# Performance work log

Measured on AMD Instinct MI355X. Metric: run time of the kernel, lower is better.

The kernel has to match this reference:

```python
import jax, jax.numpy as jnp
import numpy as np

BS, R, W, N, H = 256, 4, 128, 2048, 256
TAU, ALPHA, EPS = 1.0, 0.7, 1e-8


def _l2norm(x, axis):
    return x / (jnp.linalg.norm(x, axis=axis, keepdims=True) + EPS)


def _gumbel(u):
    # standard Gumbel(0,1) from uniform samples
    return -jnp.log(-jnp.log(u + 1e-10) + 1e-10)


def setup_inputs() -> dict:
    key = jax.random.key(0)
    ks = jax.random.split(key, 10)
    return {
        "k_r": jax.random.normal(ks[0], (BS, R * W), jnp.float32),
        "m_t": jax.random.normal(ks[1], (BS, W), jnp.float32),
        "hx": jax.random.normal(ks[2], (1, BS, H), jnp.float32),
        "memory": jax.random.uniform(ks[3], (BS, W, N), jnp.float32),
        "usage": jax.random.uniform(ks[4], (BS, N), jnp.float32),
        "read_weights": jax.random.uniform(ks[5], (BS, R, N), jnp.float32),
        "Wg": jax.random.normal(ks[6], (H, 1), jnp.float32) / np.float32(np.sqrt(H)),
        "bg": jnp.zeros((1,), jnp.float32),
        "noise_write": jax.random.uniform(ks[7], (BS, 1, N), jnp.float32),
        "noise_read": jax.random.uniform(ks[8], (BS, R, N), jnp.float32),
        "m_idx": jax.random.randint(ks[9], (BS, N), 0, N).astype(jnp.int64),
        "seq_idx": N,
    }


def reference(k_r, m_t, hx, memory, usage, read_weights, Wg, bg,
              noise_write, noise_read, m_idx, seq_idx):
    # --- key / candidate preprocessing ---
    read_keys = jnp.tanh(k_r.reshape(BS, R, W))   # bs r W
    write_m = jnp.tanh(m_t.reshape(BS, 1, W))     # bs 1 W

    # --- usage bookkeeping (read weights detached as in torch) ---
    u_t = ALPHA * usage + (1.0 - ALPHA) * jax.lax.stop_gradient(read_weights).sum(axis=1)  # bs N

    # --- write (memory-full branch: content-addressed erase/update) ---
    # reversed cosine similarity between candidate and each slot
    dist = jnp.einsum('biw,bwn->bin', _l2norm(write_m, 2), _l2norm(memory, 1))  # bs 1 N
    gamma = jax.nn.sigmoid(hx[-1] @ Wg + bg)                                    # bs 1
    soft_wt = -dist + (gamma * u_t)[:, None, :]                                 # bs 1 N
    write_wt = jax.nn.softmax((1.0 - soft_wt + _gumbel(noise_write)) / TAU, axis=2)  # bs 1 N

    m_erased = jnp.einsum('bin,bwn->biw', write_wt, memory)                     # bs 1 W
    # M * (E - e^T w) + m^T w  with e = ones -> M*(1 - w) + m^T w
    mem_new = memory * (1.0 - write_wt) + jnp.einsum('biw,bin->bwn', write_m, write_wt)
    usage_new = u_t * (1.0 - jax.lax.stop_gradient(write_wt[:, 0, :]))          # bs N

    # --- read (gumbel-softmax content addressing on updated memory) ---
    dist_r = jnp.einsum('brw,bwn->brn', _l2norm(read_keys, 2), _l2norm(mem_new, 1))  # bs r N
    read_wt = jax.nn.softmax((dist_r + _gumbel(noise_read)) / TAU, axis=2)           # bs r N
    m_read = jnp.einsum('brn,bwn->brw', read_wt, mem_new)                            # bs r W

    return (m_read, mem_new, usage_new, read_wt, m_erased)
```

## Files before the change

### kernel.cpp

```cpp
#include <hip/hip_runtime.h>

#define BS   256
#define RR   4
#define WW   128
#define NN   2048
#define HH   256
#define NT   512
#define WH   64
#define NWAVE (NT / 64)
#define RPW  (WH / NWAVE)

typedef float nfloat4 __attribute__((ext_vector_type(4)));

__device__ __forceinline__ float wave_sum(float v) {
#pragma unroll
  for (int m = 32; m >= 1; m >>= 1) v += __shfl_xor(v, m, 64);
  return v;
}
__device__ __forceinline__ float wave_max(float v) {
#pragma unroll
  for (int m = 32; m >= 1; m >>= 1) v = fmaxf(v, __shfl_xor(v, m, 64));
  return v;
}
__device__ __forceinline__ float block_sum(float v, float* s_red) {
  const int tid = threadIdx.x;
  v = wave_sum(v);
  __syncthreads();
  if ((tid & 63) == 0) s_red[tid >> 6] = v;
  __syncthreads();
  float s = s_red[0];
#pragma unroll
  for (int i = 1; i < NWAVE; ++i) s += s_red[i];
  return s;
}
__device__ __forceinline__ float block_max(float v, float* s_red) {
  const int tid = threadIdx.x;
  v = wave_max(v);
  __syncthreads();
  if ((tid & 63) == 0) s_red[tid >> 6] = v;
  __syncthreads();
  float s = s_red[0];
#pragma unroll
  for (int i = 1; i < NWAVE; ++i) s = fmaxf(s, s_red[i]);
  return s;
}
__device__ __forceinline__ void block_max4(float v[RR], float* s_red4) {
  const int tid = threadIdx.x, lane = tid & 63, wid = tid >> 6;
#pragma unroll
  for (int m = 32; m >= 1; m >>= 1) {
#pragma unroll
    for (int r = 0; r < RR; ++r) v[r] = fmaxf(v[r], __shfl_xor(v[r], m, 64));
  }
  __syncthreads();
  if (lane == 0) {
#pragma unroll
    for (int r = 0; r < RR; ++r) s_red4[wid * RR + r] = v[r];
  }
  __syncthreads();
#pragma unroll
  for (int r = 0; r < RR; ++r) {
    float s = s_red4[r];
#pragma unroll
    for (int i = 1; i < NWAVE; ++i) s = fmaxf(s, s_red4[i * RR + r]);
    v[r] = s;
  }
}
__device__ __forceinline__ void block_sum4(float v[RR], float* s_red4) {
  const int tid = threadIdx.x, lane = tid & 63, wid = tid >> 6;
#pragma unroll
  for (int m = 32; m >= 1; m >>= 1) {
#pragma unroll
    for (int r = 0; r < RR; ++r) v[r] += __shfl_xor(v[r], m, 64);
  }
  __syncthreads();
  if (lane == 0) {
#pragma unroll
    for (int r = 0; r < RR; ++r) s_red4[wid * RR + r] = v[r];
  }
  __syncthreads();
#pragma unroll
  for (int r = 0; r < RR; ++r) {
    float s = s_red4[r];
#pragma unroll
    for (int i = 1; i < NWAVE; ++i) s += s_red4[i * RR + r];
    v[r] = s;
  }
}
__device__ __forceinline__ float gumbelf(float u) {
  return -logf(-logf(u + 1e-10f) + 1e-10f);
}

#define STAT(base, rh, comp, b) ((base) + ((size_t)((rh)*6 + (comp)) * BS + (b)) * NN)

__global__ __launch_bounds__(NT, 4) void k1_stats(
    const float* __restrict__ k_r, const float* __restrict__ m_t,
    const float* __restrict__ memory, float* __restrict__ stats)
{
  __shared__ float s_wm[WH];
  __shared__ float s_rk[RR][WH];
  const int bid = blockIdx.x;
  const int b = bid >> 1, rh = bid & 1;
  const int tid = threadIdx.x;
  const int c0 = 4 * tid;

  if (tid < WH) {
    s_wm[tid] = tanhf(m_t[(size_t)b * WW + rh * WH + tid]);
  } else if (tid < WH + RR * WH) {
    const int i = tid - WH;
    s_rk[i >> 6][i & 63] =
        tanhf(k_r[(size_t)b * RR * WW + (i >> 6) * WW + rh * WH + (i & 63)]);
  }
  __syncthreads();

  const float* Mb = memory + (size_t)b * WW * NN + (size_t)rh * WH * NN;
  float cn[4] = {0.f, 0.f, 0.f, 0.f}, wd[4] = {0.f, 0.f, 0.f, 0.f};
  float rdM[RR][4];
#pragma unroll
  for (int r = 0; r < RR; ++r) {
#pragma unroll
    for (int j = 0; j < 4; ++j) rdM[r][j] = 0.f;
  }
#pragma unroll 8
  for (int w = 0; w < WH; ++w) {
    float4 v = *reinterpret_cast<const float4*>(Mb + (size_t)w * NN + c0);
    const float wmw = s_wm[w];
    cn[0] = fmaf(v.x, v.x, cn[0]); wd[0] = fmaf(wmw, v.x, wd[0]);
    cn[1] = fmaf(v.y, v.y, cn[1]); wd[1] = fmaf(wmw, v.y, wd[1]);
    cn[2] = fmaf(v.z, v.z, cn[2]); wd[2] = fmaf(wmw, v.z, wd[2]);
    cn[3] = fmaf(v.w, v.w, cn[3]); wd[3] = fmaf(wmw, v.w, wd[3]);
#pragma unroll
    for (int r = 0; r < RR; ++r) {
      const float rkw = s_rk[r][w];
      rdM[r][0] = fmaf(rkw, v.x, rdM[r][0]);
      rdM[r][1] = fmaf(rkw, v.y, rdM[r][1]);
      rdM[r][2] = fmaf(rkw, v.z, rdM[r][2]);
      rdM[r][3] = fmaf(rkw, v.w, rdM[r][3]);
    }
  }
  float4 o;
  o.x = cn[0]; o.y = cn[1]; o.z = cn[2]; o.w = cn[3];
  *reinterpret_cast<float4*>(STAT(stats, rh, 0, b) + c0) = o;
  o.x = wd[0]; o.y = wd[1]; o.z = wd[2]; o.w = wd[3];
  *reinterpret_cast<float4*>(STAT(stats, rh, 1, b) + c0) = o;
#pragma unroll
  for (int r = 0; r < RR; ++r) {
    o.x = rdM[r][0]; o.y = rdM[r][1]; o.z = rdM[r][2]; o.w = rdM[r][3];
    *reinterpret_cast<float4*>(STAT(stats, rh, 2 + r, b) + c0) = o;
  }
}

__global__ __launch_bounds__(NT) void k2_softmax(
    const float* __restrict__ k_r, const float* __restrict__ m_t,
    const float* __restrict__ hx, const float* __restrict__ usage,
    const float* __restrict__ read_weights, const float* __restrict__ Wg,
    const float* __restrict__ bg, const float* __restrict__ noise_write,
    const float* __restrict__ noise_read, const float* __restrict__ stats,
    float* __restrict__ wt_out, float* __restrict__ usage_new,
    float* __restrict__ read_wt_out)
{
  __shared__ float s_wm[WW];
  __shared__ float s_rk[RR * WW];
  __shared__ float s_red[NWAVE * RR];
  __shared__ float s_rkinv[RR], s_rkwm[RR];

  const int b = blockIdx.x;
  const int tid = threadIdx.x;
  const int lane = tid & 63;
  const int wid = tid >> 6;
  const int c0 = 4 * tid;

  float gp = 0.f;
  if (tid < HH) gp = hx[(size_t)b * HH + tid] * Wg[tid];
  if (tid < WW) s_wm[tid] = tanhf(m_t[(size_t)b * WW + tid]);
  s_rk[tid] = tanhf(k_r[(size_t)b * (RR * WW) + tid]);

  float ut[4];
  {
    const size_t rb = (size_t)b * RR * NN;
    float4 u4 = *reinterpret_cast<const float4*>(usage + (size_t)b * NN + c0);
    float4 r0 = *reinterpret_cast<const float4*>(read_weights + rb + c0);
    float4 r1 = *reinterpret_cast<const float4*>(read_weights + rb + NN + c0);
    float4 r2 = *reinterpret_cast<const float4*>(read_weights + rb + 2 * NN + c0);
    float4 r3 = *reinterpret_cast<const float4*>(read_weights + rb + 3 * NN + c0);
    ut[0] = 0.7f * u4.x + 0.3f * (r0.x + r1.x + r2.x + r3.x);
    ut[1] = 0.7f * u4.y + 0.3f * (r0.y + r1.y + r2.y + r3.y);
    ut[2] = 0.7f * u4.z + 0.3f * (r0.z + r1.z + r2.z + r3.z);
    ut[3] = 0.7f * u4.w + 0.3f * (r0.w + r1.w + r2.w + r3.w);
  }

  const float gamma = 1.f / (1.f + expf(-(block_sum(gp, s_red) + bg[0])));
  float wmp = (tid < WW) ? s_wm[tid] * s_wm[tid] : 0.f;
  const float wmss = block_sum(wmp, s_red);
  const float inv_wm = 1.f / (sqrtf(wmss) + 1e-8f);

  if (wid < RR) {
    const float a = s_rk[wid * WW + lane];
    const float c = s_rk[wid * WW + 64 + lane];
    const float wa = s_wm[lane], wc = s_wm[64 + lane];
    float ss = wave_sum(a * a + c * c);
    float sw = wave_sum(a * wa + c * wc);
    if (lane == 0) {
      s_rkinv[wid] = 1.f / (sqrtf(ss) + 1e-8f);
      s_rkwm[wid] = sw;
    }
  }
  __syncthreads();

  float cn[4], wd[4], rdM[RR][4];
  {
    float4 a0 = *reinterpret_cast<const float4*>(STAT(stats, 0, 0, b) + c0);
    float4 a1 = *reinterpret_cast<const float4*>(STAT(stats, 1, 0, b) + c0);
    cn[0] = a0.x + a1.x; cn[1] = a0.y + a1.y; cn[2] = a0.z + a1.z; cn[3] = a0.w + a1.w;
    float4 b0 = *reinterpret_cast<const float4*>(STAT(stats, 0, 1, b) + c0);
    float4 b1 = *reinterpret_cast<const float4*>(STAT(stats, 1, 1, b) + c0);
    wd[0] = b0.x + b1.x; wd[1] = b0.y + b1.y; wd[2] = b0.z + b1.z; wd[3] = b0.w + b1.w;
#pragma unroll
    for (int r = 0; r < RR; ++r) {
      float4 d0 = *reinterpret_cast<const float4*>(STAT(stats, 0, 2 + r, b) + c0);
      float4 d1 = *reinterpret_cast<const float4*>(STAT(stats, 1, 2 + r, b) + c0);
      rdM[r][0] = d0.x + d1.x; rdM[r][1] = d0.y + d1.y;
      rdM[r][2] = d0.z + d1.z; rdM[r][3] = d0.w + d1.w;
    }
  }

  float lg[4], mx = -1e30f;
  {
    float4 nw = *reinterpret_cast<const float4*>(noise_write + (size_t)b * NN + c0);
    const float nwv[4] = {nw.x, nw.y, nw.z, nw.w};
#pragma unroll
    for (int j = 0; j < 4; ++j) {
      float dist = wd[j] * inv_wm / (sqrtf(cn[j]) + 1e-8f);
      lg[j] = 1.f + dist - gamma * ut[j] + gumbelf(nwv[j]);
      mx = fmaxf(mx, lg[j]);
    }
  }
  mx = block_max(mx, s_red);
  float ex[4], es = 0.f;
#pragma unroll
  for (int j = 0; j < 4; ++j) { ex[j] = expf(lg[j] - mx); es += ex[j]; }
  es = block_sum(es, s_red);
  const float inv_es = 1.f / es;
  float wtk[4], omw[4];
#pragma unroll
  for (int j = 0; j < 4; ++j) { wtk[j] = ex[j] * inv_es; omw[j] = 1.f - wtk[j]; }
  {
    float4 un, wo;
    un.x = ut[0] * omw[0]; un.y = ut[1] * omw[1];
    un.z = ut[2] * omw[2]; un.w = ut[3] * omw[3];
    *reinterpret_cast<float4*>(usage_new + (size_t)b * NN + c0) = un;
    wo.x = wtk[0]; wo.y = wtk[1]; wo.z = wtk[2]; wo.w = wtk[3];
    *reinterpret_cast<float4*>(wt_out + (size_t)b * NN + c0) = wo;
  }

  const float invrk[RR] = { s_rkinv[0], s_rkinv[1], s_rkinv[2], s_rkinv[3] };
  const float rkwm[RR]  = { s_rkwm[0], s_rkwm[1], s_rkwm[2], s_rkwm[3] };
  float inv_cn2[4];
#pragma unroll
  for (int j = 0; j < 4; ++j) {
    float cn2 = omw[j] * omw[j] * cn[j]
              + 2.f * omw[j] * wtk[j] * wd[j]
              + wtk[j] * wtk[j] * wmss;
    inv_cn2[j] = 1.f / (sqrtf(cn2) + 1e-8f);
  }
  float lr[RR][4], mr[RR];
#pragma unroll
  for (int r = 0; r < RR; ++r) {
    float4 nr = *reinterpret_cast<const float4*>(
        noise_read + ((size_t)b * RR + r) * NN + c0);
    const float nrv[4] = {nr.x, nr.y, nr.z, nr.w};
    float m = -1e30f;
#pragma unroll
    for (int j = 0; j < 4; ++j) {
      float rd = omw[j] * rdM[r][j] + wtk[j] * rkwm[r];
      lr[r][j] = rd * invrk[r] * inv_cn2[j] + gumbelf(nrv[j]);
      m = fmaxf(m, lr[r][j]);
    }
    mr[r] = m;
  }
  block_max4(mr, s_red);
  float er[RR][4], ers[RR];
#pragma unroll
  for (int r = 0; r < RR; ++r) {
    float s = 0.f;
#pragma unroll
    for (int j = 0; j < 4; ++j) { er[r][j] = expf(lr[r][j] - mr[r]); s += er[r][j]; }
    ers[r] = s;
  }
  block_sum4(ers, s_red);
#pragma unroll
  for (int r = 0; r < RR; ++r) {
    const float inv_ers = 1.f / ers[r];
    float4 o;
    o.x = er[r][0] * inv_ers; o.y = er[r][1] * inv_ers;
    o.z = er[r][2] * inv_ers; o.w = er[r][3] * inv_ers;
    *reinterpret_cast<float4*>(read_wt_out + ((size_t)b * RR + r) * NN + c0) = o;
  }
}

__global__ __launch_bounds__(NT, 2) void k3_apply(
    const float* __restrict__ m_t, const float* __restrict__ memory,
    const float* __restrict__ wt_in, const float* __restrict__ read_wt,
    float* __restrict__ mem_new, float* __restrict__ m_read,
    float* __restrict__ m_erased)
{
  __shared__ float s_wt[NN];
  __shared__ float s_rwt[RR][NN];

  const int bid = blockIdx.x;
  const int b = bid >> 1, rh = bid & 1;
  const int tid = threadIdx.x;
  const int lane = tid & 63;
  const int wid = tid >> 6;

  {
    const int c = 4 * tid;
    float4 w4 = *reinterpret_cast<const float4*>(wt_in + (size_t)b * NN + c);
    *reinterpret_cast<float4*>(&s_wt[c]) = w4;
#pragma unroll
    for (int r = 0; r < RR; ++r) {
      float4 t = *reinterpret_cast<const float4*>(
          read_wt + ((size_t)b * RR + r) * NN + c);
      *reinterpret_cast<float4*>(&s_rwt[r][c]) = t;
    }
  }
  const int w0 = wid * RPW;
  float wm[RPW];
#pragma unroll
  for (int i = 0; i < RPW; ++i)
    wm[i] = tanhf(m_t[(size_t)b * WW + rh * WH + w0 + i]);
  __syncthreads();

  const size_t hbase = (size_t)b * WW * NN + (size_t)rh * WH * NN;
  const float* Mb = memory + hbase;
  float* MNb = mem_new + hbase;

  float pme[RPW];
  float mrp[RPW][RR];
#pragma unroll
  for (int i = 0; i < RPW; ++i) {
    pme[i] = 0.f;
#pragma unroll
    for (int r = 0; r < RR; ++r) mrp[i][r] = 0.f;
  }

#pragma unroll 1
  for (int ch = 0; ch < NN; ch += 256) {
    const int c = ch + 4 * lane;
    const float4 wt4 = *reinterpret_cast<const float4*>(&s_wt[c]);
    const float ow0 = 1.f - wt4.x, ow1 = 1.f - wt4.y,
                ow2 = 1.f - wt4.z, ow3 = 1.f - wt4.w;
    float4 rw[RR];
#pragma unroll
    for (int r = 0; r < RR; ++r)
      rw[r] = *reinterpret_cast<const float4*>(&s_rwt[r][c]);

#pragma unroll
    for (int i = 0; i < RPW; ++i) {
      const size_t off = (size_t)(w0 + i) * NN + c;
      float4 v = *reinterpret_cast<const float4*>(Mb + off);
      float4 nv;
      nv.x = fmaf(v.x, ow0, wm[i] * wt4.x);
      nv.y = fmaf(v.y, ow1, wm[i] * wt4.y);
      nv.z = fmaf(v.z, ow2, wm[i] * wt4.z);
      nv.w = fmaf(v.w, ow3, wm[i] * wt4.w);
      nfloat4 nvv;
      nvv.x = nv.x; nvv.y = nv.y; nvv.z = nv.z; nvv.w = nv.w;
      __builtin_nontemporal_store(nvv, reinterpret_cast<nfloat4*>(MNb + off));
      float p = wt4.x * v.x;
      p = fmaf(wt4.y, v.y, p);
      p = fmaf(wt4.z, v.z, p);
      p = fmaf(wt4.w, v.w, p);
      pme[i] += p;
#pragma unroll
      for (int r = 0; r < RR; ++r) {
        float a = rw[r].x * nv.x;
        a = fmaf(rw[r].y, nv.y, a);
        a = fmaf(rw[r].z, nv.z, a);
        a = fmaf(rw[r].w, nv.w, a);
        mrp[i][r] += a;
      }
    }
  }

#pragma unroll
  for (int m = 32; m >= 1; m >>= 1) {
#pragma unroll
    for (int i = 0; i < RPW; ++i) {
      pme[i] += __shfl_xor(pme[i], m, 64);
#pragma unroll
      for (int r = 0; r < RR; ++r) mrp[i][r] += __shfl_xor(mrp[i][r], m, 64);
    }
  }
  if (lane == 0) {
    const int wg = rh * WH + w0;
#pragma unroll
    for (int i = 0; i < RPW; ++i) {
      m_erased[(size_t)b * WW + wg + i] = pme[i];
#pragma unroll
      for (int r = 0; r < RR; ++r)
        m_read[(size_t)b * RR * WW + r * WW + wg + i] = mrp[i][r];
    }
  }
}

extern "C" void kernel_launch(void* const* d_in, const int* in_sizes, int n_in,
                              void* d_out, int out_size, void* d_ws, size_t ws_size,
                              hipStream_t stream) {
  (void)in_sizes; (void)n_in; (void)ws_size; (void)out_size;
  const float* k_r          = (const float*)d_in[0];
  const float* m_t          = (const float*)d_in[1];
  const float* hx           = (const float*)d_in[2];
  const float* memory       = (const float*)d_in[3];
  const float* usage        = (const float*)d_in[4];
  const float* read_weights = (const float*)d_in[5];
  const float* Wg           = (const float*)d_in[6];
  const float* bg           = (const float*)d_in[7];
  const float* noise_write  = (const float*)d_in[8];
  const float* noise_read   = (const float*)d_in[9];

  float* out       = (float*)d_out;
  float* m_read    = out;
  float* mem_new   = m_read + (size_t)BS * RR * WW;
  float* usage_new = mem_new + (size_t)BS * WW * NN;
  float* read_wt   = usage_new + (size_t)BS * NN;
  float* m_erased  = read_wt + (size_t)BS * RR * NN;

  float* stats = mem_new;
  float* wt_ws = (float*)d_ws;

  k1_stats<<<dim3(2 * BS), dim3(NT), 0, stream>>>(k_r, m_t, memory, stats);
  k2_softmax<<<dim3(BS), dim3(NT), 0, stream>>>(
      k_r, m_t, hx, usage, read_weights, Wg, bg, noise_write, noise_read,
      stats, wt_ws, usage_new, read_wt);
  k3_apply<<<dim3(2 * BS), dim3(NT), 0, stream>>>(
      m_t, memory, wt_ws, read_wt, mem_new, m_read, m_erased);
}
```

Baseline: 170.3 us.

## Fuse memory statistics pass into softmax kernel to drop stats round-trip

```diff
diff --git a/kernel.cpp b/kernel.cpp
--- a/kernel.cpp
+++ b/kernel.cpp
@@ -90,71 +90,12 @@
   return -logf(-logf(u + 1e-10f) + 1e-10f);
 }
 
-#define STAT(base, rh, comp, b) ((base) + ((size_t)((rh)*6 + (comp)) * BS + (b)) * NN)
-
-__global__ __launch_bounds__(NT, 4) void k1_stats(
+__global__ __launch_bounds__(NT) void k12_stats_softmax(
     const float* __restrict__ k_r, const float* __restrict__ m_t,
-    const float* __restrict__ memory, float* __restrict__ stats)
-{
-  __shared__ float s_wm[WH];
-  __shared__ float s_rk[RR][WH];
-  const int bid = blockIdx.x;
-  const int b = bid >> 1, rh = bid & 1;
-  const int tid = threadIdx.x;
-  const int c0 = 4 * tid;
-
-  if (tid < WH) {
-    s_wm[tid] = tanhf(m_t[(size_t)b * WW + rh * WH + tid]);
-  } else if (tid < WH + RR * WH) {
-    const int i = tid - WH;
-    s_rk[i >> 6][i & 63] =
-        tanhf(k_r[(size_t)b * RR * WW + (i >> 6) * WW + rh * WH + (i & 63)]);
-  }
-  __syncthreads();
-
-  const float* Mb = memory + (size_t)b * WW * NN + (size_t)rh * WH * NN;
-  float cn[4] = {0.f, 0.f, 0.f, 0.f}, wd[4] = {0.f, 0.f, 0.f, 0.f};
-  float rdM[RR][4];
-#pragma unroll
-  for (int r = 0; r < RR; ++r) {
-#pragma unroll
-    for (int j = 0; j < 4; ++j) rdM[r][j] = 0.f;
-  }
-#pragma unroll 8
-  for (int w = 0; w < WH; ++w) {
-    float4 v = *reinterpret_cast<const float4*>(Mb + (size_t)w * NN + c0);
-    const float wmw = s_wm[w];
-    cn[0] = fmaf(v.x, v.x, cn[0]); wd[0] = fmaf(wmw, v.x, wd[0]);
-    cn[1] = fmaf(v.y, v.y, cn[1]); wd[1] = fmaf(wmw, v.y, wd[1]);
-    cn[2] = fmaf(v.z, v.z, cn[2]); wd[2] = fmaf(wmw, v.z, wd[2]);
-    cn[3] = fmaf(v.w, v.w, cn[3]); wd[3] = fmaf(wmw, v.w, wd[3]);
-#pragma unroll
-    for (int r = 0; r < RR; ++r) {
-      const float rkw = s_rk[r][w];
-      rdM[r][0] = fmaf(rkw, v.x, rdM[r][0]);
-      rdM[r][1] = fmaf(rkw, v.y, rdM[r][1]);
-      rdM[r][2] = fmaf(rkw, v.z, rdM[r][2]);
-      rdM[r][3] = fmaf(rkw, v.w, rdM[r][3]);
-    }
-  }
-  float4 o;
-  o.x = cn[0]; o.y = cn[1]; o.z = cn[2]; o.w = cn[3];
-  *reinterpret_cast<float4*>(STAT(stats, rh, 0, b) + c0) = o;
-  o.x = wd[0]; o.y = wd[1]; o.z = wd[2]; o.w = wd[3];
-  *reinterpret_cast<float4*>(STAT(stats, rh, 1, b) + c0) = o;
-#pragma unroll
-  for (int r = 0; r < RR; ++r) {
-    o.x = rdM[r][0]; o.y = rdM[r][1]; o.z = rdM[r][2]; o.w = rdM[r][3];
-    *reinterpret_cast<float4*>(STAT(stats, rh, 2 + r, b) + c0) = o;
-  }
-}
-
-__global__ __launch_bounds__(NT) void k2_softmax(
-    const float* __restrict__ k_r, const float* __restrict__ m_t,
-    const float* __restrict__ hx, const float* __restrict__ usage,
-    const float* __restrict__ read_weights, const float* __restrict__ Wg,
-    const float* __restrict__ bg, const float* __restrict__ noise_write,
-    const float* __restrict__ noise_read, const float* __restrict__ stats,
+    const float* __restrict__ hx, const float* __restrict__ memory,
+    const float* __restrict__ usage, const float* __restrict__ read_weights,
+    const float* __restrict__ Wg, const float* __restrict__ bg,
+    const float* __restrict__ noise_write, const float* __restrict__ noise_read,
     float* __restrict__ wt_out, float* __restrict__ usage_new,
     float* __restrict__ read_wt_out)
 {
@@ -206,20 +147,30 @@
   }
   __syncthreads();
 
-  float cn[4], wd[4], rdM[RR][4];
-  {
-    float4 a0 = *reinterpret_cast<const float4*>(STAT(stats, 0, 0, b) + c0);
-    float4 a1 = *reinterpret_cast<const float4*>(STAT(stats, 1, 0, b) + c0);
-    cn[0] = a0.x + a1.x; cn[1] = a0.y + a1.y; cn[2] = a0.z + a1.z; cn[3] = a0.w + a1.w;
-    float4 b0 = *reinterpret_cast<const float4*>(STAT(stats, 0, 1, b) + c0);
-    float4 b1 = *reinterpret_cast<const float4*>(STAT(stats, 1, 1, b) + c0);
-    wd[0] = b0.x + b1.x; wd[1] = b0.y + b1.y; wd[2] = b0.z + b1.z; wd[3] = b0.w + b1.w;
+  const size_t base = (size_t)b * WW * NN;
+  const float* Mb = memory + base;
+  float cn[4] = {0.f, 0.f, 0.f, 0.f}, wd[4] = {0.f, 0.f, 0.f, 0.f};
+  float rd[RR][4];
+#pragma unroll
+  for (int r = 0; r < RR; ++r) {
+#pragma unroll
+    for (int j = 0; j < 4; ++j) rd[r][j] = 0.f;
+  }
+#pragma unroll 8
+  for (int w = 0; w < WW; ++w) {
+    float4 v = *reinterpret_cast<const float4*>(Mb + (size_t)w * NN + c0);
+    const float wmw = s_wm[w];
+    cn[0] = fmaf(v.x, v.x, cn[0]); wd[0] = fmaf(wmw, v.x, wd[0]);
+    cn[1] = fmaf(v.y, v.y, cn[1]); wd[1] = fmaf(wmw, v.y, wd[1]);
+    cn[2] = fmaf(v.z, v.z, cn[2]); wd[2] = fmaf(wmw, v.z, wd[2]);
+    cn[3] = fmaf(v.w, v.w, cn[3]); wd[3] = fmaf(wmw, v.w, wd[3]);
 #pragma unroll
     for (int r = 0; r < RR; ++r) {
-      float4 d0 = *reinterpret_cast<const float4*>(STAT(stats, 0, 2 + r, b) + c0);
-      float4 d1 = *reinterpret_cast<const float4*>(STAT(stats, 1, 2 + r, b) + c0);
-      rdM[r][0] = d0.x + d1.x; rdM[r][1] = d0.y + d1.y;
-      rdM[r][2] = d0.z + d1.z; rdM[r][3] = d0.w + d1.w;
+      const float rkw = s_rk[r * WW + w];
+      rd[r][0] = fmaf(rkw, v.x, rd[r][0]);
+      rd[r][1] = fmaf(rkw, v.y, rd[r][1]);
+      rd[r][2] = fmaf(rkw, v.z, rd[r][2]);
+      rd[r][3] = fmaf(rkw, v.w, rd[r][3]);
     }
   }
 
@@ -271,8 +222,8 @@
     float m = -1e30f;
 #pragma unroll
     for (int j = 0; j < 4; ++j) {
-      float rd = omw[j] * rdM[r][j] + wtk[j] * rkwm[r];
-      lr[r][j] = rd * invrk[r] * inv_cn2[j] + gumbelf(nrv[j]);
+      float rdn = omw[j] * rd[r][j] + wtk[j] * rkwm[r];
+      lr[r][j] = rdn * invrk[r] * inv_cn2[j] + gumbelf(nrv[j]);
       m = fmaxf(m, lr[r][j]);
     }
     mr[r] = m;
@@ -425,13 +376,11 @@
   float* read_wt   = usage_new + (size_t)BS * NN;
   float* m_erased  = read_wt + (size_t)BS * RR * NN;
 
-  float* stats = mem_new;
   float* wt_ws = (float*)d_ws;
 
-  k1_stats<<<dim3(2 * BS), dim3(NT), 0, stream>>>(k_r, m_t, memory, stats);
-  k2_softmax<<<dim3(BS), dim3(NT), 0, stream>>>(
-      k_r, m_t, hx, usage, read_weights, Wg, bg, noise_write, noise_read,
-      stats, wt_ws, usage_new, read_wt);
+  k12_stats_softmax<<<dim3(BS), dim3(NT), 0, stream>>>(
+      k_r, m_t, hx, memory, usage, read_weights, Wg, bg,
+      noise_write, noise_read, wt_ws, usage_new, read_wt);
   k3_apply<<<dim3(2 * BS), dim3(NT), 0, stream>>>(
       m_t, memory, wt_ws, read_wt, mem_new, m_read, m_erased);
 }
```

After: 162.5 us. 4.6% less time.
